# Optimization experiments

Hardware: AMD Instinct MI355X
Metric: run time of the kernel (lower is better)

## Reference

```python
import math
import jax, jax.numpy as jnp
import numpy as np

B, L, D, H = 256, 32, 512, 512
NEG_INF = -1e9


def setup_inputs() -> dict:
    key = jax.random.key(0)
    ks = jax.random.split(key, 7)
    x = jax.random.normal(ks[0], (B, L, D), dtype=jnp.float32)
    length = jax.random.randint(ks[1], (B,), 2, L + 1)  # valid lengths in [2, L]
    # word_linear: D -> 2H
    W_word = jax.random.normal(ks[2], (2 * H, D), dtype=jnp.float32) * (1.0 / math.sqrt(D))
    b_word = jnp.zeros((2 * H,), dtype=jnp.float32)
    # comp_linear: 2H -> 5H (orthogonal-ish init; scale is fine for a reference)
    W_comp = jax.random.normal(ks[3], (5 * H, 2 * H), dtype=jnp.float32) * (1.0 / math.sqrt(2 * H))
    b_comp = jnp.zeros((5 * H,), dtype=jnp.float32)
    comp_query = jax.random.normal(ks[4], (H,), dtype=jnp.float32) * 0.01
    return {"x": x, "length": length, "W_word": W_word, "b_word": b_word,
            "W_comp": W_comp, "b_comp": b_comp, "comp_query": comp_query}


def _treelstm_compose(hl, cl, hr, cr, W_comp, b_comp):
    # hl/hr: [B, n, H] -> parent h, c: [B, n, H]
    v = jnp.einsum('bnd,kd->bnk', jnp.concatenate([hl, hr], axis=2), W_comp) + b_comp
    i, fl, fr, u, o = jnp.split(v, 5, axis=2)
    c = cl * jax.nn.sigmoid(fl + 1.0) + cr * jax.nn.sigmoid(fr + 1.0) \
        + jnp.tanh(u) * jax.nn.sigmoid(i)
    h = jax.nn.sigmoid(o) * jnp.tanh(c)
    return h, c


def reference(x, length, W_word, b_word, W_comp, b_comp, comp_query):
    length_mask = (jnp.arange(L)[None, :] < length[:, None]).astype(jnp.float32)  # [B, L]
    # leaf states from word_linear (use_leaf_rnn=False path)
    hc = jnp.einsum('bld,kd->blk', x, W_word) + b_word  # [B, L, 2H]
    h, c = jnp.split(hc, 2, axis=2)
    scale = 1.0 / math.sqrt(H)
    for i in range(L - 1):
        new_h, new_c = _treelstm_compose(h[:, :-1], c[:, :-1], h[:, 1:], c[:, 1:], W_comp, b_comp)
        if i < L - 2:
            # eval-mode greedy composition selection (basic.greedy_select)
            logits = jnp.sum(comp_query * new_h, axis=-1) * scale  # [B, L-1-i]
            mask = length_mask[:, i + 1:]
            logits = jnp.where(mask > 0, logits, NEG_INF)
            select = jax.nn.one_hot(jnp.argmax(logits, axis=1), logits.shape[1], dtype=jnp.float32)
            cum = jnp.cumsum(select, axis=1)
            left = (1.0 - cum)[:, :, None]
            right = (cum - select)[:, :, None]
            sel = select[:, :, None]
            new_h = sel * new_h + left * h[:, :-1] + right * h[:, 1:]
            new_c = sel * new_c + left * c[:, :-1] + right * c[:, 1:]
        done = length_mask[:, i + 1][:, None, None]
        h = done * new_h + (1.0 - done) * h[:, :-1]
        c = done * new_c + (1.0 - done) * c[:, :-1]
    return h[:, 0, :]  # final root hidden state [B, H]
```

## Files before the change

kernel.cpp:

```cpp
#include <hip/hip_runtime.h>
#include <cmath>

#define B_   256
#define L_   32
#define H_   512
#define NH5  2560
#define N2   5120
#define SCALE 0.044194173824159216f

__device__ float g_h [B_*L_*H_];
__device__ float g_c [B_*L_*H_];
__device__ float g_al[(size_t)B_*L_*NH5];
__device__ float g_ar[(size_t)B_*L_*NH5];
__device__ float g_logit[B_*L_];
__device__ int   g_list[B_*L_];
__device__ int   g_count[B_];
__device__ int   g_merged[B_];
__device__ int   g_mpos[B_];
__device__ int   g_off[B_];
__device__ int   g_rows[B_*L_];
__device__ int   g_nrows;
__device__ int   g_mlist[2][B_];
__device__ int   g_cnt[2];

__device__ __forceinline__ float sigm(float x) { return 1.0f / (1.0f + expf(-x)); }

__global__ __launch_bounds__(256) void init_all(const int* __restrict__ length) {
  __shared__ int sw[4];
  const int t = threadIdx.x;
  const int len = length[t];
  int v = len;
#pragma unroll
  for (int off = 1; off < 64; off <<= 1) {
    int o = __shfl_up(v, off, 64);
    if ((t & 63) >= off) v += o;
  }
  if ((t & 63) == 63) sw[t >> 6] = v;
  __syncthreads();
  int base = 0;
  for (int w = 0; w < (t >> 6); w++) base += sw[w];
  const int incl = base + v;
  const int off0 = incl - len;
  g_off[t] = off0;
  if (t == 255) g_nrows = incl;
  g_count[t] = len; g_merged[t] = -2; g_mpos[t] = 0;
  if (t == 0) { g_cnt[0] = 0; g_cnt[1] = 0; }
#pragma unroll
  for (int s = 0; s < L_; s++) g_list[t*L_ + s] = s;
  for (int s = 0; s < len; s++) g_rows[off0 + s] = t*L_ + s;
}

template<int MODE>
__global__ __launch_bounds__(256) void gemm_big(
    const float* __restrict__ Aext,
    const float* __restrict__ Bm,
    const float* __restrict__ bias)
{
  const int NR = g_nrows;
  const int m0 = blockIdx.x * 128;
  if (m0 >= NR) return;
  const int n0 = blockIdx.y * 128;

  const int tid = threadIdx.x;
  const int w = tid >> 6, l = tid & 63;
  const int tx = (w & 1) * 8 + (l & 7);
  const int ty = (w >> 1) * 8 + (l >> 3);

  __shared__ float As[2][16][128];
  __shared__ float Bs[2][16][128];

  const int ra = tid >> 1, qa = (tid & 1) * 8;

  const float* Abase = (MODE == 0) ? Aext : g_h;
  int mr = m0 + ra; if (mr >= NR) mr = NR - 1;
  const float* aptr = Abase + (size_t)g_rows[mr] * 512 + qa;

  const float* bptr;
  {
    int nrow = n0 + ra;
    if (MODE == 0) bptr = Bm + (size_t)nrow * 512 + qa;
    else bptr = Bm + (nrow < NH5 ? (size_t)nrow * 1024
                                 : (size_t)(nrow - NH5) * 1024 + 512) + qa;
  }

  float4 a0 = *(const float4*)(aptr),     a1 = *(const float4*)(aptr + 4);
  float4 b0 = *(const float4*)(bptr),     b1 = *(const float4*)(bptr + 4);
  float acc[8][8] = {};

  for (int k0 = 0; k0 < 512; k0 += 16) {
    const int buf = (k0 >> 4) & 1;
    As[buf][qa+0][ra]=a0.x; As[buf][qa+1][ra]=a0.y; As[buf][qa+2][ra]=a0.z; As[buf][qa+3][ra]=a0.w;
    As[buf][qa+4][ra]=a1.x; As[buf][qa+5][ra]=a1.y; As[buf][qa+6][ra]=a1.z; As[buf][qa+7][ra]=a1.w;
    Bs[buf][qa+0][ra]=b0.x; Bs[buf][qa+1][ra]=b0.y; Bs[buf][qa+2][ra]=b0.z; Bs[buf][qa+3][ra]=b0.w;
    Bs[buf][qa+4][ra]=b1.x; Bs[buf][qa+5][ra]=b1.y; Bs[buf][qa+6][ra]=b1.z; Bs[buf][qa+7][ra]=b1.w;
    __syncthreads();
    if (k0 + 16 < 512) {
      a0 = *(const float4*)(aptr + k0 + 16); a1 = *(const float4*)(aptr + k0 + 20);
      b0 = *(const float4*)(bptr + k0 + 16); b1 = *(const float4*)(bptr + k0 + 20);
    }
#pragma unroll
    for (int k = 0; k < 16; k++) {
      float af[8], bf[8];
#pragma unroll
      for (int c = 0; c < 2; c++) {
        float4 t = *(const float4*)&As[buf][k][ty*8 + 4*c];
        af[4*c+0]=t.x; af[4*c+1]=t.y; af[4*c+2]=t.z; af[4*c+3]=t.w;
      }
#pragma unroll
      for (int c = 0; c < 2; c++) {
        float4 t = *(const float4*)&Bs[buf][k][tx*8 + 4*c];
        bf[4*c+0]=t.x; bf[4*c+1]=t.y; bf[4*c+2]=t.z; bf[4*c+3]=t.w;
      }
#pragma unroll
      for (int i = 0; i < 8; i++)
#pragma unroll
        for (int j = 0; j < 8; j++)
          acc[i][j] = fmaf(af[i], bf[j], acc[i][j]);
    }
  }

  const int nb = n0 + tx*8;
  float4 bias_lo, bias_hi;
  if (MODE == 0) { bias_lo = *(const float4*)(bias + nb);
                   bias_hi = *(const float4*)(bias + nb + 4); }
#pragma unroll
  for (int i = 0; i < 8; i++) {
    int mrow = m0 + ty*8 + i;
    if (mrow >= NR) continue;
    int crow = g_rows[mrow];
    float4 v0 = make_float4(acc[i][0], acc[i][1], acc[i][2], acc[i][3]);
    float4 v1 = make_float4(acc[i][4], acc[i][5], acc[i][6], acc[i][7]);
    if (MODE == 0) {
      v0.x += bias_lo.x; v0.y += bias_lo.y; v0.z += bias_lo.z; v0.w += bias_lo.w;
      v1.x += bias_hi.x; v1.y += bias_hi.y; v1.z += bias_hi.z; v1.w += bias_hi.w;
      float* dst = (nb < H_) ? g_h + (size_t)crow*H_ + nb
                             : g_c + (size_t)crow*H_ + (nb - H_);
      *(float4*)(dst) = v0; *(float4*)(dst + 4) = v1;
    } else {
      float* dst = (nb < NH5) ? g_al + (size_t)crow*NH5 + nb
                              : g_ar + (size_t)crow*NH5 + (nb - NH5);
      *(float4*)(dst) = v0; *(float4*)(dst + 4) = v1;
    }
  }
}

__global__ __launch_bounds__(256) void iter0_logits(const int* __restrict__ length,
                                                    const float* __restrict__ bc,
                                                    const float* __restrict__ qv) {
  __shared__ float sred[4];
  const int p = blockIdx.x, b = blockIdx.y;
  if (p >= length[b] - 1) return;
  const float* al = g_al + (size_t)(b*L_ + p)*NH5;
  const float* ar = g_ar + (size_t)(b*L_ + p + 1)*NH5;
  const float* cl = g_c  + (size_t)(b*L_ + p)*H_;
  const float* cr = g_c  + (size_t)(b*L_ + p + 1)*H_;
  float part = 0.f;
#pragma unroll
  for (int jj = 0; jj < H_/256; jj++) {
    int j = threadIdx.x + jj*256;
    float vi  = al[j]       + ar[j]       + bc[j];
    float vfl = al[H_+j]    + ar[H_+j]    + bc[H_+j];
    float vfr = al[2*H_+j]  + ar[2*H_+j]  + bc[2*H_+j];
    float vu  = al[3*H_+j]  + ar[3*H_+j]  + bc[3*H_+j];
    float vo  = al[4*H_+j]  + ar[4*H_+j]  + bc[4*H_+j];
    float c = cl[j]*sigm(vfl+1.f) + cr[j]*sigm(vfr+1.f) + tanhf(vu)*sigm(vi);
    float h = sigm(vo)*tanhf(c);
    part = fmaf(qv[j], h, part);
  }
#pragma unroll
  for (int off = 32; off; off >>= 1) part += __shfl_down(part, off, 64);
  if ((threadIdx.x & 63) == 0) sred[threadIdx.x >> 6] = part;
  __syncthreads();
  if (threadIdx.x == 0)
    g_logit[b*L_ + p] = (sred[0]+sred[1]+sred[2]+sred[3]) * SCALE;
}

__global__ __launch_bounds__(256) void select_merge(int iter,
    const int* __restrict__ length,
    const float* __restrict__ bc,
    const float* __restrict__ qv,
    float* __restrict__ out)
{
  __shared__ float sred[4];
  __shared__ int s_sel[3];
  const int b = blockIdx.x, tid = threadIdx.x;
  if (b == 0 && tid == 0) g_cnt[(iter & 1) ^ 1] = 0;

  const int m     = g_count[b];
  const int pslot = g_merged[b];
  const int ppos  = g_mpos[b];
  int* list = g_list + b*L_;

  if (iter > 0 && pslot >= 0) {
    const int half = tid >> 7, lt = tid & 127;
    int sl = -1, sr = -1;
    if (half == 0) { if (ppos > 0)     { sl = list[ppos-1]; sr = list[ppos];   } }
    else           { if (ppos < m - 1) { sl = list[ppos];   sr = list[ppos+1]; } }
    float part = 0.f;
    if (sl >= 0) {
      const float* al = g_al + (size_t)(b*L_+sl)*NH5;
      const float* ar = g_ar + (size_t)(b*L_+sr)*NH5;
      const float* cl = g_c  + (size_t)(b*L_+sl)*H_;
      const float* cr = g_c  + (size_t)(b*L_+sr)*H_;
      const int j = lt * 4;
      float4 ai  = *(const float4*)(al + j)        , bi  = *(const float4*)(ar + j);
      float4 afl = *(const float4*)(al + H_   + j) , bfl = *(const float4*)(ar + H_   + j);
      float4 afr = *(const float4*)(al + 2*H_ + j) , bfr = *(const float4*)(ar + 2*H_ + j);
      float4 au  = *(const float4*)(al + 3*H_ + j) , bu  = *(const float4*)(ar + 3*H_ + j);
      float4 ao  = *(const float4*)(al + 4*H_ + j) , bo  = *(const float4*)(ar + 4*H_ + j);
      float4 c4l = *(const float4*)(cl + j)        , c4r = *(const float4*)(cr + j);
      float4 q4  = *(const float4*)(qv + j);
      const float* bc0 = bc + j;
      float c, h;
      c = c4l.x*sigm(afl.x+bfl.x+bc0[H_]+1.f)   + c4r.x*sigm(afr.x+bfr.x+bc0[2*H_]+1.f)
        + tanhf(au.x+bu.x+bc0[3*H_])*sigm(ai.x+bi.x+bc0[0]);
      h = sigm(ao.x+bo.x+bc0[4*H_])*tanhf(c);   part = fmaf(q4.x, h, part);
      c = c4l.y*sigm(afl.y+bfl.y+bc0[H_+1]+1.f) + c4r.y*sigm(afr.y+bfr.y+bc0[2*H_+1]+1.f)
        + tanhf(au.y+bu.y+bc0[3*H_+1])*sigm(ai.y+bi.y+bc0[1]);
      h = sigm(ao.y+bo.y+bc0[4*H_+1])*tanhf(c); part = fmaf(q4.y, h, part);
      c = c4l.z*sigm(afl.z+bfl.z+bc0[H_+2]+1.f) + c4r.z*sigm(afr.z+bfr.z+bc0[2*H_+2]+1.f)
        + tanhf(au.z+bu.z+bc0[3*H_+2])*sigm(ai.z+bi.z+bc0[2]);
      h = sigm(ao.z+bo.z+bc0[4*H_+2])*tanhf(c); part = fmaf(q4.z, h, part);
      c = c4l.w*sigm(afl.w+bfl.w+bc0[H_+3]+1.f) + c4r.w*sigm(afr.w+bfr.w+bc0[2*H_+3]+1.f)
        + tanhf(au.w+bu.w+bc0[3*H_+3])*sigm(ai.w+bi.w+bc0[3]);
      h = sigm(ao.w+bo.w+bc0[4*H_+3])*tanhf(c); part = fmaf(q4.w, h, part);
    }
#pragma unroll
    for (int off = 32; off; off >>= 1) part += __shfl_down(part, off, 64);
    if ((tid & 63) == 0) sred[tid >> 6] = part;
    __syncthreads();
    if (tid == 0   && ppos > 0)     g_logit[b*L_ + list[ppos-1]] = (sred[0]+sred[1])*SCALE;
    if (tid == 128 && ppos < m - 1) g_logit[b*L_ + list[ppos]]   = (sred[2]+sred[3])*SCALE;
  }

  const bool active = iter < (length[b] - 1);
  if (active) {
    __syncthreads();

    if (tid < 64) {
      float lg = -1e30f; int idx = tid;
      if (tid < m - 1) lg = g_logit[b*L_ + list[tid]];
#pragma unroll
      for (int off = 32; off; off >>= 1) {
        float olg = __shfl_down(lg, off, 64);
        int   oid = __shfl_down(idx, off, 64);
        if (olg > lg || (olg == lg && oid < idx)) { lg = olg; idx = oid; }
      }
      if (tid == 0) { s_sel[0] = idx; s_sel[1] = list[idx]; s_sel[2] = list[idx+1]; }
    }
    __syncthreads();
    const int pos = s_sel[0], sl = s_sel[1], sr = s_sel[2];

    if (tid < 128) {
      const float* al = g_al + (size_t)(b*L_+sl)*NH5;
      const float* ar = g_ar + (size_t)(b*L_+sr)*NH5;
      float*       cl = g_c  + (size_t)(b*L_+sl)*H_;
      const float* cr = g_c  + (size_t)(b*L_+sr)*H_;
      float*       hl = g_h  + (size_t)(b*L_+sl)*H_;
      const int j = tid * 4;
      float4 ai  = *(const float4*)(al + j)        , bi  = *(const float4*)(ar + j);
      float4 afl = *(const float4*)(al + H_   + j) , bfl = *(const float4*)(ar + H_   + j);
      float4 afr = *(const float4*)(al + 2*H_ + j) , bfr = *(const float4*)(ar + 2*H_ + j);
      float4 au  = *(const float4*)(al + 3*H_ + j) , bu  = *(const float4*)(ar + 3*H_ + j);
      float4 ao  = *(const float4*)(al + 4*H_ + j) , bo  = *(const float4*)(ar + 4*H_ + j);
      float4 c4l = *(const float4*)(cl + j)        , c4r = *(const float4*)(cr + j);
      const float* bc0 = bc + j;
      float4 cn, hn;
      cn.x = c4l.x*sigm(afl.x+bfl.x+bc0[H_]+1.f)   + c4r.x*sigm(afr.x+bfr.x+bc0[2*H_]+1.f)
           + tanhf(au.x+bu.x+bc0[3*H_])*sigm(ai.x+bi.x+bc0[0]);
      hn.x = sigm(ao.x+bo.x+bc0[4*H_])*tanhf(cn.x);
      cn.y = c4l.y*sigm(afl.y+bfl.y+bc0[H_+1]+1.f) + c4r.y*sigm(afr.y+bfr.y+bc0[2*H_+1]+1.f)
           + tanhf(au.y+bu.y+bc0[3*H_+1])*sigm(ai.y+bi.y+bc0[1]);
      hn.y = sigm(ao.y+bo.y+bc0[4*H_+1])*tanhf(cn.y);
      cn.z = c4l.z*sigm(afl.z+bfl.z+bc0[H_+2]+1.f) + c4r.z*sigm(afr.z+bfr.z+bc0[2*H_+2]+1.f)
           + tanhf(au.z+bu.z+bc0[3*H_+2])*sigm(ai.z+bi.z+bc0[2]);
      hn.z = sigm(ao.z+bo.z+bc0[4*H_+2])*tanhf(cn.z);
      cn.w = c4l.w*sigm(afl.w+bfl.w+bc0[H_+3]+1.f) + c4r.w*sigm(afr.w+bfr.w+bc0[2*H_+3]+1.f)
           + tanhf(au.w+bu.w+bc0[3*H_+3])*sigm(ai.w+bi.w+bc0[3]);
      hn.w = sigm(ao.w+bo.w+bc0[4*H_+3])*tanhf(cn.w);
      *(float4*)(cl + j) = cn;
      *(float4*)(hl + j) = hn;
    }
    __syncthreads();
    if (tid == 0) {
      for (int n = pos+1; n < m-1; n++) list[n] = list[n+1];
      g_count[b]  = m - 1;
      g_merged[b] = sl;
      g_mpos[b]   = pos;
      int k = atomicAdd(&g_cnt[iter & 1], 1);
      g_mlist[iter & 1][k] = b;
    }
  } else {
    if (tid == 0) g_merged[b] = -1;
  }

  if (iter == L_-2) {
    __syncthreads();
    for (int j = tid; j < H_; j += 256)
      out[(size_t)b*H_ + j] = g_h[(size_t)(b*L_)*H_ + j];
  }
}

__global__ __launch_bounds__(256) void gemm_iter(int par, const float* __restrict__ Wc)
{
  const int nact = g_cnt[par];
  const int m0 = blockIdx.y * 32;
  if (m0 >= nact) return;
  const int n0 = blockIdx.x * 64;
  const int tid = threadIdx.x;

  __shared__ float As[32][32];
  __shared__ float Bs[32][64];

  const int ra = tid >> 3, qa = (tid & 7) * 4;
  int mr = m0 + ra; if (mr >= nact) mr = nact - 1;
  const int bbA = g_mlist[par][mr];
  const float* aptr = g_h + (size_t)(bbA*L_ + g_merged[bbA]) * 512 + qa;

  const int rb = tid >> 2, qb = (tid & 3) * 8;
  const int nr = n0 + rb;
  const float* bptr = (nr < NH5) ? Wc + (size_t)nr * 1024 + qb
                                 : Wc + (size_t)(nr - NH5) * 1024 + 512 + qb;

  const int tx = tid & 15, ty = tid >> 4;

  float4 av  = *(const float4*)(aptr);
  float4 bv0 = *(const float4*)(bptr);
  float4 bv1 = *(const float4*)(bptr + 4);
  float acc[2][4] = {};

  for (int k0 = 0; k0 < 512; k0 += 32) {
    __syncthreads();
    As[qa+0][ra] = av.x;  As[qa+1][ra] = av.y;  As[qa+2][ra] = av.z;  As[qa+3][ra] = av.w;
    Bs[qb+0][rb] = bv0.x; Bs[qb+1][rb] = bv0.y; Bs[qb+2][rb] = bv0.z; Bs[qb+3][rb] = bv0.w;
    Bs[qb+4][rb] = bv1.x; Bs[qb+5][rb] = bv1.y; Bs[qb+6][rb] = bv1.z; Bs[qb+7][rb] = bv1.w;
    __syncthreads();
    if (k0 + 32 < 512) {
      av  = *(const float4*)(aptr + k0 + 32);
      bv0 = *(const float4*)(bptr + k0 + 32);
      bv1 = *(const float4*)(bptr + k0 + 36);
    }
#pragma unroll
    for (int k = 0; k < 32; k++) {
      float2 a2 = *(const float2*)&As[k][ty*2];
      float4 b4 = *(const float4*)&Bs[k][tx*4];
      acc[0][0] = fmaf(a2.x, b4.x, acc[0][0]);
      acc[0][1] = fmaf(a2.x, b4.y, acc[0][1]);
      acc[0][2] = fmaf(a2.x, b4.z, acc[0][2]);
      acc[0][3] = fmaf(a2.x, b4.w, acc[0][3]);
      acc[1][0] = fmaf(a2.y, b4.x, acc[1][0]);
      acc[1][1] = fmaf(a2.y, b4.y, acc[1][1]);
      acc[1][2] = fmaf(a2.y, b4.z, acc[1][2]);
      acc[1][3] = fmaf(a2.y, b4.w, acc[1][3]);
    }
  }

#pragma unroll
  for (int i = 0; i < 2; i++) {
    int mrow = m0 + ty*2 + i;
    if (mrow >= nact) continue;
    int bb = g_mlist[par][mrow];
    size_t base = (size_t)(bb*L_ + g_merged[bb]) * NH5;
    int n = n0 + tx*4;
    float4 v = make_float4(acc[i][0], acc[i][1], acc[i][2], acc[i][3]);
    if (n < NH5) *(float4*)(g_al + base + n)         = v;
    else         *(float4*)(g_ar + base + (n - NH5)) = v;
  }
}

extern "C" void kernel_launch(void* const* d_in, const int* in_sizes, int n_in,
                              void* d_out, int out_size, void* d_ws, size_t ws_size,
                              hipStream_t stream)
{
  (void)in_sizes; (void)n_in; (void)out_size; (void)d_ws; (void)ws_size;
  const float* x      = (const float*)d_in[0];
  const int*   length = (const int*)  d_in[1];
  const float* W_word = (const float*)d_in[2];
  const float* b_word = (const float*)d_in[3];
  const float* W_comp = (const float*)d_in[4];
  const float* b_comp = (const float*)d_in[5];
  const float* q      = (const float*)d_in[6];
  float* out = (float*)d_out;

  init_all<<<1, 256, 0, stream>>>(length);

  gemm_big<0><<<dim3(64, 1024/128), 256, 0, stream>>>(x, W_word, b_word);
  gemm_big<1><<<dim3(64, N2/128),   256, 0, stream>>>(nullptr, W_comp, nullptr);

  iter0_logits<<<dim3(L_-1, B_), 256, 0, stream>>>(length, b_comp, q);

  for (int i = 0; i < L_-1; i++) {
    select_merge<<<B_, 256, 0, stream>>>(i, length, b_comp, q, out);
    if (i < L_-2)
      gemm_iter<<<dim3(N2/64, 8), 256, 0, stream>>>(i & 1, W_comp);
  }
}
```

Baseline: 1.752 ms.

## Shrink gemm_big K-tile to 8 with single buffer and swap grid axes

The leaf and composition GEMMs now use a single-buffered 8-deep K slice (one float4 per operand per thread) instead of a double-buffered 16-deep slice, which cuts shared memory and register use per block. The grid is also transposed so that the N tiles vary fastest along blockIdx.x, meaning consecutive blocks share the same A rows. The intent is higher occupancy and better L2 reuse of the A rows. The cost is twice as many K iterations, each with two barriers, and less latency hiding between load and compute.

```diff
diff --git a/kernel.cpp b/kernel.cpp
--- a/kernel.cpp
+++ b/kernel.cpp
@@ -57,19 +57,19 @@
     const float* __restrict__ bias)
 {
   const int NR = g_nrows;
-  const int m0 = blockIdx.x * 128;
+  const int m0 = blockIdx.y * 128;
   if (m0 >= NR) return;
-  const int n0 = blockIdx.y * 128;
+  const int n0 = blockIdx.x * 128;
 
   const int tid = threadIdx.x;
   const int w = tid >> 6, l = tid & 63;
   const int tx = (w & 1) * 8 + (l & 7);
   const int ty = (w >> 1) * 8 + (l >> 3);
 
-  __shared__ float As[2][16][128];
-  __shared__ float Bs[2][16][128];
-
-  const int ra = tid >> 1, qa = (tid & 1) * 8;
+  __shared__ float As[8][128];
+  __shared__ float Bs[8][128];
+
+  const int ra = tid >> 1, qa = (tid & 1) * 4;
 
   const float* Abase = (MODE == 0) ? Aext : g_h;
   int mr = m0 + ra; if (mr >= NR) mr = NR - 1;
@@ -83,32 +83,30 @@
                                  : (size_t)(nrow - NH5) * 1024 + 512) + qa;
   }
 
-  float4 a0 = *(const float4*)(aptr),     a1 = *(const float4*)(aptr + 4);
-  float4 b0 = *(const float4*)(bptr),     b1 = *(const float4*)(bptr + 4);
+  float4 av = *(const float4*)(aptr);
+  float4 bv = *(const float4*)(bptr);
   float acc[8][8] = {};
 
-  for (int k0 = 0; k0 < 512; k0 += 16) {
-    const int buf = (k0 >> 4) & 1;
-    As[buf][qa+0][ra]=a0.x; As[buf][qa+1][ra]=a0.y; As[buf][qa+2][ra]=a0.z; As[buf][qa+3][ra]=a0.w;
-    As[buf][qa+4][ra]=a1.x; As[buf][qa+5][ra]=a1.y; As[buf][qa+6][ra]=a1.z; As[buf][qa+7][ra]=a1.w;
-    Bs[buf][qa+0][ra]=b0.x; Bs[buf][qa+1][ra]=b0.y; Bs[buf][qa+2][ra]=b0.z; Bs[buf][qa+3][ra]=b0.w;
-    Bs[buf][qa+4][ra]=b1.x; Bs[buf][qa+5][ra]=b1.y; Bs[buf][qa+6][ra]=b1.z; Bs[buf][qa+7][ra]=b1.w;
-    __syncthreads();
-    if (k0 + 16 < 512) {
-      a0 = *(const float4*)(aptr + k0 + 16); a1 = *(const float4*)(aptr + k0 + 20);
-      b0 = *(const float4*)(bptr + k0 + 16); b1 = *(const float4*)(bptr + k0 + 20);
-    }
-#pragma unroll
-    for (int k = 0; k < 16; k++) {
+  for (int k0 = 0; k0 < 512; k0 += 8) {
+    __syncthreads();
+    As[qa+0][ra] = av.x; As[qa+1][ra] = av.y; As[qa+2][ra] = av.z; As[qa+3][ra] = av.w;
+    Bs[qa+0][ra] = bv.x; Bs[qa+1][ra] = bv.y; Bs[qa+2][ra] = bv.z; Bs[qa+3][ra] = bv.w;
+    __syncthreads();
+    if (k0 + 8 < 512) {
+      av = *(const float4*)(aptr + k0 + 8);
+      bv = *(const float4*)(bptr + k0 + 8);
+    }
+#pragma unroll
+    for (int k = 0; k < 8; k++) {
       float af[8], bf[8];
 #pragma unroll
       for (int c = 0; c < 2; c++) {
-        float4 t = *(const float4*)&As[buf][k][ty*8 + 4*c];
+        float4 t = *(const float4*)&As[k][ty*8 + 4*c];
         af[4*c+0]=t.x; af[4*c+1]=t.y; af[4*c+2]=t.z; af[4*c+3]=t.w;
       }
 #pragma unroll
       for (int c = 0; c < 2; c++) {
-        float4 t = *(const float4*)&Bs[buf][k][tx*8 + 4*c];
+        float4 t = *(const float4*)&Bs[k][tx*8 + 4*c];
         bf[4*c+0]=t.x; bf[4*c+1]=t.y; bf[4*c+2]=t.z; bf[4*c+3]=t.w;
       }
 #pragma unroll
@@ -384,8 +382,8 @@
 
   init_all<<<1, 256, 0, stream>>>(length);
 
-  gemm_big<0><<<dim3(64, 1024/128), 256, 0, stream>>>(x, W_word, b_word);
-  gemm_big<1><<<dim3(64, N2/128),   256, 0, stream>>>(nullptr, W_comp, nullptr);
+  gemm_big<0><<<dim3(1024/128, 64), 256, 0, stream>>>(x, W_word, b_word);
+  gemm_big<1><<<dim3(N2/128,   64), 256, 0, stream>>>(nullptr, W_comp, nullptr);
 
   iter0_logits<<<dim3(L_-1, B_), 256, 0, stream>>>(length, b_comp, q);
 
```

Measured after the change: 1.686 ms. -3.8%, faster.
